# Optimization experiments

Measured on AMD Instinct MI355X. Metric: run time of the kernel, lower is better.

## Reference

```python
import jax, jax.numpy as jnp
import numpy as np

IN_DIM = 256
QK_DIM = IN_DIM // 8


def setup_inputs() -> dict:
    key = jax.random.key(0)
    ks = jax.random.split(key, 10)
    B, C, W, H = 4, IN_DIM, 64, 64
    a = jax.random.normal(ks[0], (B, C, W, H), dtype=jnp.float32)
    b = jax.random.normal(ks[1], (B, C, W, H), dtype=jnp.float32)
    c = jax.random.uniform(ks[2], (B, 1, 2 * W, 2 * H), dtype=jnp.float32)
    scale = 0.02
    wq = jax.random.normal(ks[3], (QK_DIM, C), dtype=jnp.float32) * scale
    bq = jnp.zeros((QK_DIM,), dtype=jnp.float32)
    wk = jax.random.normal(ks[4], (QK_DIM, C), dtype=jnp.float32) * scale
    bk = jnp.zeros((QK_DIM,), dtype=jnp.float32)
    wv = jax.random.normal(ks[5], (C, C), dtype=jnp.float32) * scale
    bv = jnp.zeros((C,), dtype=jnp.float32)
    gamma = jnp.ones((1,), dtype=jnp.float32)
    return {"a": a, "b": b, "c": c, "wq": wq, "bq": bq, "wk": wk,
            "bk": bk, "wv": wv, "bv": bv, "gamma": gamma}


def reference(a, b, c, wq, bq, wk, bk, wv, bv, gamma):
    B, C, W, H = a.shape
    N = W * H
    # F.interpolate(c, scale_factor=1/down_rate, mode='nearest'): output idx i -> input idx i*down_rate
    down = c.shape[2] // W
    cd = c[:, :, ::down, ::down]                      # [B,1,W,H]
    # 1x1 convs as channel contractions
    q = jnp.einsum('bchw,oc->bohw', a, wq) + bq[None, :, None, None]
    k = jnp.einsum('bchw,oc->bohw', b, wk) + bk[None, :, None, None]
    v = jnp.einsum('bchw,oc->bohw', a, wv) + bv[None, :, None, None]
    qf = q.reshape(B, QK_DIM, N)                      # proj_query^T rows are spatial
    kf = k.reshape(B, QK_DIM, N)
    vf = v.reshape(B, C, N)
    sim = jnp.einsum('bdi,bdj->bij', qf, kf)          # [B,N,N]
    cflat = cd.reshape(B, N)
    # mask[b,i,j] = cflat[b,i] (per-query multiplicative logit scaling)
    logits = sim * cflat[:, :, None]
    attn = jax.nn.softmax(logits, axis=-1)            # [B,N,N]
    out_attn = jnp.einsum('bcj,bij->bci', vf, attn).reshape(B, C, W, H)
    out = gamma * a * cd + (1.0 - cd) * out_attn
    return out
```

## Files before the change

kernel.cpp:

```cpp
#include <hip/hip_runtime.h>

#define LOG2E 1.44269504088896340736f

typedef __attribute__((ext_vector_type(8))) short short8;
typedef __attribute__((ext_vector_type(4))) float float4v;
typedef __attribute__((ext_vector_type(2))) float float2v;
typedef __attribute__((ext_vector_type(2))) int int2v;
typedef __attribute__((ext_vector_type(4))) int int4v;

__device__ inline unsigned short f2bf(float f) {
    union { float f; unsigned u; } v; v.f = f;
    unsigned r = v.u + 0x7fffu + ((v.u >> 16) & 1u);
    return (unsigned short)(r >> 16);
}
__device__ inline float bf2f(unsigned short u) {
    union { unsigned u; float f; } v; v.u = ((unsigned)u) << 16;
    return v.f;
}
__device__ inline unsigned pk_bf16(float a, float b) {
    union { float f; unsigned u; } ua, ub; ua.f = a; ub.f = b;
    return __builtin_amdgcn_perm(ub.u + 0x8000u, ua.u + 0x8000u, 0x07060302u);
}

__global__ void wcvt_kernel(const float* __restrict__ wq, const float* __restrict__ wk,
                            const float* __restrict__ wv, unsigned short* __restrict__ Wbf)
{
    int idx = blockIdx.x * 256 + threadIdx.x;
    int e4  = idx * 4;
    int row = e4 >> 8, col = e4 & 255;
    const float* src = (row < 32) ? (wq + row * 256 + col)
                     : (row < 64) ? (wk + (row - 32) * 256 + col)
                                  : (wv + (row - 64) * 256 + col);
    float4v v = *(const float4v*)src;
    int2v p;
    p.x = (unsigned)f2bf(v[0]) | ((unsigned)f2bf(v[1]) << 16);
    p.y = (unsigned)f2bf(v[2]) | ((unsigned)f2bf(v[3]) << 16);
    *(int2v*)(Wbf + e4) = p;
}

__launch_bounds__(512, 2)
__global__ void proj_kernel(const float* __restrict__ a_p, const float* __restrict__ b_p,
                            const float* __restrict__ c_p,
                            const float* __restrict__ bq, const float* __restrict__ bk,
                            const float* __restrict__ bv,
                            const unsigned short* __restrict__ Wbf,
                            unsigned short* __restrict__ Qg, unsigned short* __restrict__ Kg,
                            unsigned short* __restrict__ Vg)
{
    __shared__ __align__(16) unsigned short At[64 * 264];
    __shared__ __align__(16) unsigned short Bt[64 * 264];
    __shared__ float bias[320];
    __shared__ float cdl[64];

    const int t    = threadIdx.x;
    const int blk  = blockIdx.x;
    const int b    = blk & 3;
    const int tile = blk >> 2;
    const int i0   = tile * 64;
    const int lane = t & 63;
    const int w    = t >> 6;
    const int q    = lane >> 4;
    const int n    = lane & 15;
    const int it   = w & 3;
    const int mh   = w >> 2;

    {
        const int arr = t >> 8, cp = (t >> 1) & 127, ih = (t & 1) * 32;
        const float* src = (arr ? b_p : a_p) + ((size_t)(b * 256 + 2 * cp)) * 4096 + i0 + ih;
        unsigned* dst = (unsigned*)(arr ? Bt : At) + cp;
#pragma unroll
        for (int h = 0; h < 4; ++h) {
            float4v r0a = *(const float4v*)(src + h * 8);
            float4v r0b = *(const float4v*)(src + h * 8 + 4);
            float4v r1a = *(const float4v*)(src + 4096 + h * 8);
            float4v r1b = *(const float4v*)(src + 4096 + h * 8 + 4);
#pragma unroll
            for (int jj = 0; jj < 4; ++jj)
                dst[(ih + h * 8 + jj) * 132] = pk_bf16(r0a[jj], r1a[jj]);
#pragma unroll
            for (int jj = 0; jj < 4; ++jj)
                dst[(ih + h * 8 + 4 + jj) * 132] = pk_bf16(r0b[jj], r1b[jj]);
        }
        if (t < 320) bias[t] = (t < 32) ? bq[t] : (t < 64) ? bk[t - 32] : bv[t - 64];
        else if (t < 384) cdl[t - 320] = c_p[b * 16384 + tile * 256 + (t - 320) * 2];
    }
    __syncthreads();

    float4v acc[10];
#pragma unroll
    for (int j = 0; j < 10; ++j) acc[j] = (float4v){0.f, 0.f, 0.f, 0.f};

#pragma unroll 2
    for (int kc = 0; kc < 8; ++kc) {
        short8 xa = *(const short8*)&At[(it * 16 + n) * 264 + kc * 32 + q * 8];
        short8 xb = xa;
        if (mh == 0)
            xb = *(const short8*)&Bt[(it * 16 + n) * 264 + kc * 32 + q * 8];
#pragma unroll
        for (int j = 0; j < 10; ++j) {
            int mt = mh * 10 + j;
            short8 wf = *(const short8*)(Wbf + (size_t)(mt * 16 + n) * 256 + kc * 32 + q * 8);
            short8 bsel = (mt == 2 || mt == 3) ? xb : xa;
            acc[j] = __builtin_amdgcn_mfma_f32_16x16x32_bf16(wf, bsel, acc[j], 0, 0, 0);
        }
    }
    __syncthreads();

    unsigned short* QKst = At;
    unsigned short* Vst  = Bt;
    {
        const float cdq = cdl[it * 16 + n] * LOG2E;
#pragma unroll
        for (int j = 0; j < 10; ++j) {
            int mt = mh * 10 + j;
            float4v bv4 = *(const float4v*)&bias[mt * 16 + q * 4];
            float v0 = acc[j][0] + bv4[0], v1 = acc[j][1] + bv4[1];
            float v2 = acc[j][2] + bv4[2], v3 = acc[j][3] + bv4[3];
            if (mt < 2) {
                v0 *= cdq; v1 *= cdq; v2 *= cdq; v3 *= cdq;
                int2v pk; pk.x = (int)pk_bf16(v0, v1); pk.y = (int)pk_bf16(v2, v3);
                *(int2v*)&QKst[(it * 16 + n) * 72 + mt * 16 + q * 4] = pk;
            } else if (mt < 4) {
                int2v pk; pk.x = (int)pk_bf16(v0, v1); pk.y = (int)pk_bf16(v2, v3);
                *(int2v*)&QKst[(it * 16 + n) * 72 + mt * 16 + q * 4] = pk;
            } else {
                int p = ((n >> 2) * 8) + ((it & 1) * 4) + (n & 3);
                int cbase = mt * 16 - 64 + q * 4;
                int jb = it >> 1;
                Vst[((jb * 256) + cbase + 0) * 32 + p] = f2bf(v0);
                Vst[((jb * 256) + cbase + 1) * 32 + p] = f2bf(v1);
                Vst[((jb * 256) + cbase + 2) * 32 + p] = f2bf(v2);
                Vst[((jb * 256) + cbase + 3) * 32 + p] = f2bf(v3);
            }
        }
    }
    __syncthreads();

    {
        int i = t >> 3, h8 = t & 7;
        int4v v = *(const int4v*)&QKst[i * 72 + h8 * 8];
        unsigned short* dstp = (h8 < 4)
            ? Qg + (size_t)(b * 4096 + i0 + i) * 32 + h8 * 8
            : Kg + (size_t)(b * 4096 + i0 + i) * 32 + (h8 - 4) * 8;
        *(int4v*)dstp = v;
    }
    {
#pragma unroll
        for (int k = 0; k < 4; ++k) {
            int flat = k * 512 + t;
            int4v v = *(const int4v*)&Vst[flat * 8];
            int jb = flat >> 10;
            *(int4v*)(Vg + (size_t)(b * 128 + tile * 2 + jb) * 8192 + (flat & 1023) * 8) = v;
        }
    }
}

__launch_bounds__(256, 3)
__global__ void attn_kernel(const unsigned short* __restrict__ Qg,
                            const unsigned short* __restrict__ Kg,
                            const unsigned short* __restrict__ Vg,
                            unsigned short* __restrict__ Opart, float* __restrict__ lsum)
{
    const int t    = threadIdx.x;
    const int blk  = blockIdx.x;
    const int b    = blk & 3;
    const int s_lo = (blk >> 2) & 1;
    const int rt   = (blk >> 3) & 63;
    const int s    = s_lo + 2 * (blk >> 9);
    const int lidx = (s << 8) | (rt << 2) | b;
    const int i0   = rt * 64;
    const int lane = t & 63;
    const int w    = t >> 6;
    const int q    = lane >> 4;
    const int n    = lane & 15;

    short8 qf[4];
#pragma unroll
    for (int ig = 0; ig < 4; ++ig)
        qf[ig] = *(const short8*)(Qg + (size_t)(b * 4096 + i0 + ig * 16 + n) * 32 + q * 8);

    float4v acc[4][4];
#pragma unroll
    for (int ig = 0; ig < 4; ++ig)
#pragma unroll
        for (int ct = 0; ct < 4; ++ct) acc[ig][ct] = (float4v){0.f, 0.f, 0.f, 0.f};
    float lsc[4] = {0.f, 0.f, 0.f, 0.f};

    const float4v m16v = (float4v){-16.f, -16.f, -16.f, -16.f};

    const unsigned short* kb = Kg + (size_t)(b * 4096 + s * 1024 + n) * 32 + q * 8;
    const unsigned short* vb = Vg + ((size_t)((b * 128 + s * 32) * 256 + w * 64 + n)) * 32 + q * 8;

    short8 kf0 = *(const short8*)(kb);
    short8 kf1 = *(const short8*)(kb + 512);

#pragma unroll 1
    for (int it = 0; it < 32; ++it) {
        short8 vf[4];
#pragma unroll
        for (int ct = 0; ct < 4; ++ct)
            vf[ct] = *(const short8*)(vb + ct * 512);

        short8 pf[4];
#pragma unroll
        for (int ig = 0; ig < 4; ++ig) {
            float4v s0 = __builtin_amdgcn_mfma_f32_16x16x32_bf16(kf0, qf[ig], m16v, 0, 0, 0);
            float4v s1 = __builtin_amdgcn_mfma_f32_16x16x32_bf16(kf1, qf[ig], m16v, 0, 0, 0);
            float p0 = __builtin_amdgcn_exp2f(s0[0]), p1 = __builtin_amdgcn_exp2f(s0[1]);
            float p2 = __builtin_amdgcn_exp2f(s0[2]), p3 = __builtin_amdgcn_exp2f(s0[3]);
            float p4 = __builtin_amdgcn_exp2f(s1[0]), p5 = __builtin_amdgcn_exp2f(s1[1]);
            float p6 = __builtin_amdgcn_exp2f(s1[2]), p7 = __builtin_amdgcn_exp2f(s1[3]);
            lsc[ig] += ((p0 + p1) + (p2 + p3)) + ((p4 + p5) + (p6 + p7));
            union { short8 s8; unsigned u[4]; } pf_;
            pf_.u[0] = pk_bf16(p0, p1);
            pf_.u[1] = pk_bf16(p2, p3);
            pf_.u[2] = pk_bf16(p4, p5);
            pf_.u[3] = pk_bf16(p6, p7);
            pf[ig] = pf_.s8;
        }

        kf0 = *(const short8*)(kb + 1024);
        kf1 = *(const short8*)(kb + 1536);

#pragma unroll
        for (int ig = 0; ig < 4; ++ig)
#pragma unroll
            for (int ct = 0; ct < 4; ++ct)
                acc[ig][ct] = __builtin_amdgcn_mfma_f32_16x16x32_bf16(pf[ig], vf[ct], acc[ig][ct], 0, 0, 0);

        kb += 1024;
        vb += 8192;
    }

    const size_t obase = (size_t)lidx * 16384;
#pragma unroll
    for (int ig = 0; ig < 4; ++ig)
#pragma unroll
        for (int ct = 0; ct < 4; ++ct) {
            int c = w * 64 + ct * 16 + n;
            int i = ig * 16 + q * 4;
            int2v pk;
            pk.x = (int)pk_bf16(acc[ig][ct][0], acc[ig][ct][1]);
            pk.y = (int)pk_bf16(acc[ig][ct][2], acc[ig][ct][3]);
            *(int2v*)(Opart + obase + (size_t)c * 64 + i) = pk;
        }
#pragma unroll
    for (int ig = 0; ig < 4; ++ig) {
        float v = lsc[ig];
        v += __shfl_xor(v, 16, 64);
        v += __shfl_xor(v, 32, 64);
        if (w == 0 && lane < 16)
            lsum[(size_t)lidx * 64 + ig * 16 + lane] = v;
    }
}

__launch_bounds__(256, 4)
__global__ void combine_kernel(const float* __restrict__ a_p, const float* __restrict__ c_p,
                               const float* __restrict__ gamma_p,
                               const unsigned short* __restrict__ Opart,
                               const float* __restrict__ lsum, float* __restrict__ out)
{
    __shared__ float invL[64];
    __shared__ float cdl[64];

    const int t   = threadIdx.x;
    const int blk = blockIdx.x;
    const int b   = blk & 3;
    const int rt  = (blk >> 2) & 63;
    const int cs  = blk >> 8;
    const int i0  = rt * 64;

    if (t < 64) {
        float L = 0.f;
#pragma unroll
        for (int s = 0; s < 4; ++s)
            L += lsum[(size_t)((s << 8) | (rt << 2) | b) * 64 + t];
        invL[t] = 1.0f / L;
        cdl[t] = c_p[b * 16384 + rt * 256 + 2 * t];
    }
    __syncthreads();

    const float gam = gamma_p[0];
    const int il = (t & 31) * 2;
    const int cq = t >> 5;
#pragma unroll
    for (int k = 0; k < 4; ++k) {
        int c = cs * 32 + cq + 8 * k;
        float o0 = 0.f, o1 = 0.f;
#pragma unroll
        for (int s = 0; s < 4; ++s) {
            int idx = (s << 8) | (rt << 2) | b;
            unsigned pr = *(const unsigned*)(Opart + (size_t)idx * 16384 + (size_t)c * 64 + il);
            o0 += bf2f((unsigned short)(pr & 0xffff));
            o1 += bf2f((unsigned short)(pr >> 16));
        }
        o0 *= invL[il];
        o1 *= invL[il + 1];
        size_t gi = (size_t)(b * 256 + c) * 4096 + i0 + il;
        float2v av = *(const float2v*)(a_p + gi);
        float cd0 = cdl[il], cd1 = cdl[il + 1];
        float2v ov;
        ov[0] = gam * av[0] * cd0 + (1.0f - cd0) * o0;
        ov[1] = gam * av[1] * cd1 + (1.0f - cd1) * o1;
        *(float2v*)(out + gi) = ov;
    }
}

extern "C" void kernel_launch(void* const* d_in, const int* in_sizes, int n_in,
                              void* d_out, int out_size, void* d_ws, size_t ws_size,
                              hipStream_t stream)
{
    const float* a_p   = (const float*)d_in[0];
    const float* b_p   = (const float*)d_in[1];
    const float* c_p   = (const float*)d_in[2];
    const float* wq    = (const float*)d_in[3];
    const float* bq    = (const float*)d_in[4];
    const float* wk    = (const float*)d_in[5];
    const float* bk    = (const float*)d_in[6];
    const float* wv    = (const float*)d_in[7];
    const float* bv    = (const float*)d_in[8];
    const float* gamma = (const float*)d_in[9];
    float* out = (float*)d_out;

    unsigned short* Qg    = (unsigned short*)d_ws;
    unsigned short* Kg    = Qg + (size_t)4 * 4096 * 32;
    unsigned short* Vg    = Kg + (size_t)4 * 4096 * 32;
    unsigned short* Wbf   = Vg + (size_t)4 * 256 * 4096;
    unsigned short* Opart = Wbf + (size_t)320 * 256;
    float*          lsum  = (float*)(Opart + (size_t)1024 * 16384);

    wcvt_kernel<<<80, 256, 0, stream>>>(wq, wk, wv, Wbf);
    proj_kernel<<<256, 512, 0, stream>>>(a_p, b_p, c_p, bq, bk, bv, Wbf, Qg, Kg, Vg);
    attn_kernel<<<1024, 256, 0, stream>>>(Qg, Kg, Vg, Opart, lsum);
    combine_kernel<<<2048, 256, 0, stream>>>(a_p, c_p, gamma, Opart, lsum, out);
}
```

Baseline: 188.4 us.

## Fuse combine into attention kernel with in-block split-K reduction via LDS

Attention blocks now cover all keys for a 64-row tile, splitting keys across two wave groups within a 512-thread block and reducing their partial outputs and row sums through shared memory. The final normalisation and blend with the input are done in the same kernel, removing the separate combine launch and the global bf16 partial buffer. The cost is a smaller grid (256 blocks), twice as many loop iterations per wave, and lower occupancy, which may reduce latency hiding.

```diff
diff --git a/kernel.cpp b/kernel.cpp
--- a/kernel.cpp
+++ b/kernel.cpp
@@ -155,24 +155,29 @@
     }
 }
 
-__launch_bounds__(256, 3)
+__launch_bounds__(512, 2)
 __global__ void attn_kernel(const unsigned short* __restrict__ Qg,
                             const unsigned short* __restrict__ Kg,
                             const unsigned short* __restrict__ Vg,
-                            unsigned short* __restrict__ Opart, float* __restrict__ lsum)
+                            const float* __restrict__ a_p, const float* __restrict__ c_p,
+                            const float* __restrict__ gamma_p, float* __restrict__ out)
 {
+    __shared__ unsigned short Obuf[256 * 68];
+    __shared__ float Lb0[64], Lb1[64], cdl[64];
+
     const int t    = threadIdx.x;
     const int blk  = blockIdx.x;
     const int b    = blk & 3;
-    const int s_lo = (blk >> 2) & 1;
-    const int rt   = (blk >> 3) & 63;
-    const int s    = s_lo + 2 * (blk >> 9);
-    const int lidx = (s << 8) | (rt << 2) | b;
+    const int rt   = blk >> 2;
     const int i0   = rt * 64;
     const int lane = t & 63;
     const int w    = t >> 6;
     const int q    = lane >> 4;
     const int n    = lane & 15;
+    const int cs   = w & 3;
+    const int h    = w >> 2;
+
+    if (t < 64) cdl[t] = c_p[b * 16384 + rt * 256 + t * 2];
 
     short8 qf[4];
 #pragma unroll
@@ -188,14 +193,14 @@
 
     const float4v m16v = (float4v){-16.f, -16.f, -16.f, -16.f};
 
-    const unsigned short* kb = Kg + (size_t)(b * 4096 + s * 1024 + n) * 32 + q * 8;
-    const unsigned short* vb = Vg + ((size_t)((b * 128 + s * 32) * 256 + w * 64 + n)) * 32 + q * 8;
+    const unsigned short* kb = Kg + (size_t)(b * 4096 + h * 2048 + n) * 32 + q * 8;
+    const unsigned short* vb = Vg + ((size_t)((b * 128 + h * 64) * 256 + cs * 64 + n)) * 32 + q * 8;
 
     short8 kf0 = *(const short8*)(kb);
     short8 kf1 = *(const short8*)(kb + 512);
 
 #pragma unroll 1
-    for (int it = 0; it < 32; ++it) {
+    for (int it = 0; it < 64; ++it) {
         short8 vf[4];
 #pragma unroll
         for (int ct = 0; ct < 4; ++ct)
@@ -232,77 +237,69 @@
         vb += 8192;
     }
 
-    const size_t obase = (size_t)lidx * 16384;
-#pragma unroll
-    for (int ig = 0; ig < 4; ++ig)
-#pragma unroll
-        for (int ct = 0; ct < 4; ++ct) {
-            int c = w * 64 + ct * 16 + n;
-            int i = ig * 16 + q * 4;
-            int2v pk;
-            pk.x = (int)pk_bf16(acc[ig][ct][0], acc[ig][ct][1]);
-            pk.y = (int)pk_bf16(acc[ig][ct][2], acc[ig][ct][3]);
-            *(int2v*)(Opart + obase + (size_t)c * 64 + i) = pk;
-        }
+    float lred[4];
 #pragma unroll
     for (int ig = 0; ig < 4; ++ig) {
         float v = lsc[ig];
         v += __shfl_xor(v, 16, 64);
         v += __shfl_xor(v, 32, 64);
-        if (w == 0 && lane < 16)
-            lsum[(size_t)lidx * 64 + ig * 16 + lane] = v;
-    }
-}
-
-__launch_bounds__(256, 4)
-__global__ void combine_kernel(const float* __restrict__ a_p, const float* __restrict__ c_p,
-                               const float* __restrict__ gamma_p,
-                               const unsigned short* __restrict__ Opart,
-                               const float* __restrict__ lsum, float* __restrict__ out)
-{
-    __shared__ float invL[64];
-    __shared__ float cdl[64];
-
-    const int t   = threadIdx.x;
-    const int blk = blockIdx.x;
-    const int b   = blk & 3;
-    const int rt  = (blk >> 2) & 63;
-    const int cs  = blk >> 8;
-    const int i0  = rt * 64;
-
-    if (t < 64) {
-        float L = 0.f;
-#pragma unroll
-        for (int s = 0; s < 4; ++s)
-            L += lsum[(size_t)((s << 8) | (rt << 2) | b) * 64 + t];
-        invL[t] = 1.0f / L;
-        cdl[t] = c_p[b * 16384 + rt * 256 + 2 * t];
+        lred[ig] = v;
+    }
+    {
+        const int cbase = cs * 64;
+        const int ct0 = h ? 0 : 2;
+#pragma unroll
+        for (int ig = 0; ig < 4; ++ig)
+#pragma unroll
+            for (int cc = 0; cc < 2; ++cc) {
+                int ct = ct0 + cc;
+                int c = cbase + ct * 16 + n;
+                int i = ig * 16 + q * 4;
+                int2v pk;
+                pk.x = (int)pk_bf16(acc[ig][ct][0], acc[ig][ct][1]);
+                pk.y = (int)pk_bf16(acc[ig][ct][2], acc[ig][ct][3]);
+                *(int2v*)&Obuf[c * 68 + i] = pk;
+            }
+        if (w == 0) {
+#pragma unroll
+            for (int ig = 0; ig < 4; ++ig) if (lane < 16) Lb0[ig * 16 + lane] = lred[ig];
+        } else if (w == 4) {
+#pragma unroll
+            for (int ig = 0; ig < 4; ++ig) if (lane < 16) Lb1[ig * 16 + lane] = lred[ig];
+        }
     }
     __syncthreads();
-
-    const float gam = gamma_p[0];
-    const int il = (t & 31) * 2;
-    const int cq = t >> 5;
-#pragma unroll
-    for (int k = 0; k < 4; ++k) {
-        int c = cs * 32 + cq + 8 * k;
-        float o0 = 0.f, o1 = 0.f;
-#pragma unroll
-        for (int s = 0; s < 4; ++s) {
-            int idx = (s << 8) | (rt << 2) | b;
-            unsigned pr = *(const unsigned*)(Opart + (size_t)idx * 16384 + (size_t)c * 64 + il);
-            o0 += bf2f((unsigned short)(pr & 0xffff));
-            o1 += bf2f((unsigned short)(pr >> 16));
-        }
-        o0 *= invL[il];
-        o1 *= invL[il + 1];
-        size_t gi = (size_t)(b * 256 + c) * 4096 + i0 + il;
-        float2v av = *(const float2v*)(a_p + gi);
-        float cd0 = cdl[il], cd1 = cdl[il + 1];
-        float2v ov;
-        ov[0] = gam * av[0] * cd0 + (1.0f - cd0) * o0;
-        ov[1] = gam * av[1] * cd1 + (1.0f - cd1) * o1;
-        *(float2v*)(out + gi) = ov;
+    {
+        const int cbase = cs * 64;
+        const int ctf = h ? 2 : 0;
+        const float gam = gamma_p[0];
+#pragma unroll
+        for (int ig = 0; ig < 4; ++ig) {
+            int ib = ig * 16 + q * 4;
+            float invL[4], cdv[4];
+#pragma unroll
+            for (int r = 0; r < 4; ++r) {
+                invL[r] = 1.0f / (Lb0[ib + r] + Lb1[ib + r]);
+                cdv[r]  = cdl[ib + r];
+            }
+#pragma unroll
+            for (int cc = 0; cc < 2; ++cc) {
+                int ct = ctf + cc;
+                int c = cbase + ct * 16 + n;
+                int2v st = *(const int2v*)&Obuf[c * 68 + ib];
+                size_t gi = ((size_t)(b * 256 + c)) * 4096 + i0 + ib;
+                float4v av = *(const float4v*)(a_p + gi);
+                float4v ov;
+#pragma unroll
+                for (int r = 0; r < 4; ++r) {
+                    unsigned pr = (r < 2) ? (unsigned)st.x : (unsigned)st.y;
+                    float part = bf2f((unsigned short)((r & 1) ? (pr >> 16) : (pr & 0xffffu)));
+                    float o = (acc[ig][ct][r] + part) * invL[r];
+                    ov[r] = gam * av[r] * cdv[r] + (1.0f - cdv[r]) * o;
+                }
+                *(float4v*)(out + gi) = ov;
+            }
+        }
     }
 }
 
@@ -322,15 +319,12 @@
     const float* gamma = (const float*)d_in[9];
     float* out = (float*)d_out;
 
-    unsigned short* Qg    = (unsigned short*)d_ws;
-    unsigned short* Kg    = Qg + (size_t)4 * 4096 * 32;
-    unsigned short* Vg    = Kg + (size_t)4 * 4096 * 32;
-    unsigned short* Wbf   = Vg + (size_t)4 * 256 * 4096;
-    unsigned short* Opart = Wbf + (size_t)320 * 256;
-    float*          lsum  = (float*)(Opart + (size_t)1024 * 16384);
+    unsigned short* Qg  = (unsigned short*)d_ws;
+    unsigned short* Kg  = Qg + (size_t)4 * 4096 * 32;
+    unsigned short* Vg  = Kg + (size_t)4 * 4096 * 32;
+    unsigned short* Wbf = Vg + (size_t)4 * 256 * 4096;
 
     wcvt_kernel<<<80, 256, 0, stream>>>(wq, wk, wv, Wbf);
     proj_kernel<<<256, 512, 0, stream>>>(a_p, b_p, c_p, bq, bk, bv, Wbf, Qg, Kg, Vg);
-    attn_kernel<<<1024, 256, 0, stream>>>(Qg, Kg, Vg, Opart, lsum);
-    combine_kernel<<<2048, 256, 0, stream>>>(a_p, c_p, gamma, Opart, lsum, out);
-}
+    attn_kernel<<<256, 512, 0, stream>>>(Qg, Kg, Vg, a_p, c_p, gamma, out);
+}
```

Result: slower. 195.5 us (+3.7%).
